# Kernel optimization log

Hardware: AMD Instinct MI355X
Metric: run time of the kernel (lower is better)

The kernel has to match this reference:

```python
import jax, jax.numpy as jnp
import numpy as np

EMBED_DIM = 1024
NUM_HEADS = 16
HEAD_DIM = EMBED_DIM // NUM_HEADS


def setup_inputs() -> dict:
    key = jax.random.key(0)
    k1, k2, k3, k4, k5 = jax.random.split(key, 5)
    B, T, C = 2, 2048, EMBED_DIM
    s = 1.0 / np.sqrt(C)
    return {
        "x": jax.random.normal(k1, (B, T, C), dtype=jnp.float32),
        "W_qkv": jax.random.normal(k2, (C, 3 * C), dtype=jnp.float32) * s,
        "b_qkv": jnp.zeros((3 * C,), dtype=jnp.float32),
        "W_out": jax.random.normal(k3, (C, C), dtype=jnp.float32) * s,
        "b_out": jnp.zeros((C,), dtype=jnp.float32),
    }


def reference(x, W_qkv, b_qkv, W_out, b_out):
    B, T, C = x.shape
    H, D = NUM_HEADS, HEAD_DIM
    qkv = x @ W_qkv + b_qkv                       # [B, T, 3C]
    q, k, v = jnp.split(qkv, 3, axis=-1)
    # [B, H, T, D]
    q = q.reshape(B, T, H, D).transpose(0, 2, 1, 3)
    k = k.reshape(B, T, H, D).transpose(0, 2, 1, 3)
    v = v.reshape(B, T, H, D).transpose(0, 2, 1, 3)
    scores = jnp.einsum("bhqd,bhkd->bhqk", q, k) / np.sqrt(D)  # [B,H,T,T]
    causal = jnp.tril(jnp.ones((T, T), dtype=bool))
    scores = jnp.where(causal[None, None], scores, -jnp.inf)
    weights = jax.nn.softmax(scores, axis=-1)
    out = jnp.einsum("bhqk,bhkd->bhqd", weights, v)  # [B,H,T,D]
    out = out.transpose(0, 2, 1, 3).reshape(B, T, C)
    return out @ W_out + b_out
```

## Files before the change

kernel.cpp:

```cpp
#include <hip/hip_runtime.h>
#include <stdint.h>

typedef unsigned short u16t;
typedef __attribute__((ext_vector_type(8))) short bf16x8;
typedef __attribute__((ext_vector_type(4))) float f32x4;

#define DEV __device__ __forceinline__

DEV u16t f2bf(float f) {
  union { float f; unsigned u; } v; v.f = f;
  unsigned r = v.u + 0x7FFFu + ((v.u >> 16) & 1u);
  return (u16t)(r >> 16);
}

DEV unsigned cvtpk(float a, float b) {
  unsigned r;
  asm("v_cvt_pk_bf16_f32 %0, %1, %2" : "=v"(r) : "v"(a), "v"(b));
  return r;
}

DEV void glds16(const void* g, void* l) {
  __builtin_amdgcn_global_load_lds((const __attribute__((address_space(1))) void*)g,
                                   (__attribute__((address_space(3))) void*)l, 16, 0, 0);
}

__global__ __launch_bounds__(256) void k_cast_x(const float* __restrict__ x,
                                                u16t* __restrict__ xb, int n) {
  int i = (blockIdx.x * 256 + threadIdx.x) * 8;
  if (i >= n) return;
  const float4* p = (const float4*)(x + i);
  float4 a = p[0], b = p[1];
  union { u16t h[8]; int4 v; } o;
  o.h[0] = f2bf(a.x); o.h[1] = f2bf(a.y); o.h[2] = f2bf(a.z); o.h[3] = f2bf(a.w);
  o.h[4] = f2bf(b.x); o.h[5] = f2bf(b.y); o.h[6] = f2bf(b.z); o.h[7] = f2bf(b.w);
  *(int4*)(xb + i) = o.v;
}

__global__ __launch_bounds__(256) void k_transpose_cast(const float* __restrict__ src,
                                                        u16t* __restrict__ dst,
                                                        int R, int C) {
  __shared__ u16t tile[64][65];
  int c0 = blockIdx.x * 64, r0 = blockIdx.y * 64;
  int tid = threadIdx.x;
#pragma unroll
  for (int i = 0; i < 16; i++) {
    int idx = tid + i * 256;
    int r = idx >> 6, c = idx & 63;
    tile[c][r] = f2bf(src[(size_t)(r0 + r) * C + (c0 + c)]);
  }
  __syncthreads();
#pragma unroll
  for (int i = 0; i < 16; i++) {
    int idx = tid + i * 256;
    int rr = idx >> 6, cc = idx & 63;
    dst[(size_t)(c0 + rr) * R + (r0 + cc)] = tile[rr][cc];
  }
}

template <int K>
DEV void gemm_mainloop(const u16t* __restrict__ A, const u16t* __restrict__ Bt,
                       int m0, int n0, u16t* ldsA, u16t* ldsB, f32x4 acc[4][4]) {
  const int tid = threadIdx.x;
  const int lane = tid & 63;
  const int wid = tid >> 6;
  const int wm = wid >> 1, wn = wid & 1;
#pragma unroll
  for (int i = 0; i < 4; i++)
#pragma unroll
    for (int j = 0; j < 4; j++) acc[i][j] = f32x4{0.f, 0.f, 0.f, 0.f};

  char* lA = (char*)ldsA;
  char* lB = (char*)ldsB;

  for (int k0 = 0; k0 < K; k0 += 32) {
#pragma unroll
    for (int j = 0; j < 2; j++) {
      int g = wid * 64 + lane + j * 256;
      int row = g >> 2;
      int cb = (g & 3) * 16;
      glds16((const char*)(A + (size_t)(m0 + row) * K + k0) + cb,
             lA + j * 4096 + wid * 1024);
      glds16((const char*)(Bt + (size_t)(n0 + row) * K + k0) + cb,
             lB + j * 4096 + wid * 1024);
    }
    __syncthreads();
    bf16x8 af[4], bfr[4];
    const int lr = lane & 15;
    const int ko = (lane >> 4) * 8;
#pragma unroll
    for (int f = 0; f < 4; f++) {
      af[f]  = *(const bf16x8*)(ldsA + (wm * 64 + f * 16 + lr) * 32 + ko);
      bfr[f] = *(const bf16x8*)(ldsB + (wn * 64 + f * 16 + lr) * 32 + ko);
    }
#pragma unroll
    for (int i = 0; i < 4; i++)
#pragma unroll
      for (int j = 0; j < 4; j++)
        acc[i][j] = __builtin_amdgcn_mfma_f32_16x16x32_bf16(af[i], bfr[j], acc[i][j], 0, 0, 0);
    __syncthreads();
  }
}

__global__ __launch_bounds__(256) void k_gemm_qkv(const u16t* __restrict__ xb,
                                                  const u16t* __restrict__ wt,
                                                  const float* __restrict__ bias,
                                                  u16t* __restrict__ q,
                                                  u16t* __restrict__ kk,
                                                  u16t* __restrict__ vt) {
  __shared__ u16t ldsA[128 * 32];
  __shared__ u16t ldsB[128 * 32];
  __shared__ u16t ldsE[4][64 * 64];
  const int m0 = blockIdx.x * 128, n0 = blockIdx.y * 128;
  f32x4 acc[4][4];
  gemm_mainloop<1024>(xb, wt, m0, n0, ldsA, ldsB, acc);

  const int lane = threadIdx.x & 63, wid = threadIdx.x >> 6;
  const int wm = wid >> 1, wn = wid & 1;
  const int nbase = n0 + wn * 64;
  const int which = nbase >> 10;
  const int hb = (nbase & 1023) >> 6;
  const int bb = m0 >> 11;
  const int t0 = (m0 & 2047) + wm * 64;
  const int bh = bb * 16 + hb;
  u16t* eb = ldsE[wid];
#pragma unroll
  for (int fm = 0; fm < 4; fm++) {
#pragma unroll
    for (int fn = 0; fn < 4; fn++) {
      float bv = bias[nbase + fn * 16 + (lane & 15)];
#pragma unroll
      for (int i = 0; i < 4; i++) {
        int t_loc = fm * 16 + (lane >> 4) * 4 + i;
        int d_loc = fn * 16 + (lane & 15);
        float v = acc[fm][fn][i] + bv;
        if (which == 2) eb[d_loc * 64 + t_loc] = f2bf(v);
        else            eb[t_loc * 64 + d_loc] = f2bf(v);
      }
    }
  }
  asm volatile("s_waitcnt lgkmcnt(0)" ::: "memory");
  u16t* dst;
  size_t base, rowstride;
  if (which == 2) { dst = vt; base = (size_t)bh * 64 * 2048 + t0; rowstride = 2048; }
  else { dst = (which == 0) ? q : kk; base = ((size_t)bh * 2048 + t0) * 64; rowstride = 64; }
#pragma unroll
  for (int it = 0; it < 8; it++) {
    int g = it * 64 + lane;
    int r = g >> 3;
    int ce = (g & 7) * 8;
    *(int4*)(dst + base + (size_t)r * rowstride + ce) = *(const int4*)(eb + r * 64 + ce);
  }
}

__global__ __launch_bounds__(128) void k_attn(const u16t* __restrict__ q,
                                              const u16t* __restrict__ kk,
                                              const u16t* __restrict__ vt,
                                              u16t* __restrict__ attn) {
  __shared__ u16t ldsK[64 * 64];
  __shared__ u16t ldsV[64 * 64];
  __shared__ u16t ldsP[2][16 * 64];
  const int p = blockIdx.x;
  const int t_lo = p, t_hi = 63 - p;
  const int lo_tiles = (t_lo >> 1) + 1;
  const int hi_tiles = (t_hi >> 1) + 1;
  const int bh = blockIdx.y;
  const int tid = threadIdx.x;
  const int lane = tid & 63, wid = tid >> 6;
  const int lr = lane & 15, lg = lane >> 4;
  const size_t hbase = (size_t)bh * 2048 * 64;
  const size_t vbase = (size_t)bh * 64 * 2048;
  const float NINF = -__builtin_inff();
  const float CEXP = 0.1803368801111204f;

  bf16x8 qlo[2], qhi[2];
  {
    const u16t* qp  = q + hbase + (size_t)(t_lo * 32 + wid * 16 + lr) * 64 + lg * 8;
    const u16t* qp2 = q + hbase + (size_t)(t_hi * 32 + wid * 16 + lr) * 64 + lg * 8;
#pragma unroll
    for (int ks = 0; ks < 2; ks++) {
      qlo[ks] = *(const bf16x8*)(qp + ks * 32);
      qhi[ks] = *(const bf16x8*)(qp2 + ks * 32);
    }
  }

  f32x4 olo[4], ohi[4];
#pragma unroll
  for (int i = 0; i < 4; i++) {
    olo[i] = f32x4{0.f, 0.f, 0.f, 0.f};
    ohi[i] = f32x4{0.f, 0.f, 0.f, 0.f};
  }
  float mlo = NINF, llo = 0.f, mhi = NINF, lhi = 0.f;

  u16t* pb = ldsP[wid];

  auto stage = [&](int kt) {
#pragma unroll
    for (int j = 0; j < 4; j++) {
      int g = j * 128 + tid;
      int r = g >> 3;
      int cb = (g & 7) * 16;
      int sc = cb ^ ((r & 7) << 4);
      glds16((const char*)(kk + hbase + (size_t)(kt * 64 + r) * 64) + sc,
             (char*)ldsK + j * 2048 + wid * 1024);
      glds16((const char*)(vt + vbase + (size_t)r * 2048 + kt * 64) + sc,
             (char*)ldsV + j * 2048 + wid * 1024);
    }
  };

  auto compute = [&](bool diag, int moff, const bf16x8* qf, f32x4* o,
                     float& m_run, float& l_run) {
    const char* K = (const char*)ldsK;
    const char* V = (const char*)ldsV;
    float sv[4][4];
    __builtin_amdgcn_s_setprio(1);
#pragma unroll
    for (int f = 0; f < 4; f++) {
      f32x4 s = f32x4{0.f, 0.f, 0.f, 0.f};
#pragma unroll
      for (int ks = 0; ks < 2; ks++) {
        int row = f * 16 + lr;
        int cb = ks * 64 + lg * 16;
        bf16x8 kf = *(const bf16x8*)(K + row * 128 + (cb ^ ((row & 7) << 4)));
        s = __builtin_amdgcn_mfma_f32_16x16x32_bf16(kf, qf[ks], s, 0, 0, 0);
      }
#pragma unroll
      for (int i = 0; i < 4; i++) sv[f][i] = s[i];
    }
    __builtin_amdgcn_s_setprio(0);
    if (diag) {
      int qr = moff + wid * 16 + lr;
#pragma unroll
      for (int f = 0; f < 4; f++)
#pragma unroll
        for (int i = 0; i < 4; i++)
          if (f * 16 + lg * 4 + i > qr) sv[f][i] = NINF;
    }
    float m0a = fmaxf(fmaxf(sv[0][0], sv[0][1]), fmaxf(sv[0][2], sv[0][3]));
    float m1a = fmaxf(fmaxf(sv[1][0], sv[1][1]), fmaxf(sv[1][2], sv[1][3]));
    float m2a = fmaxf(fmaxf(sv[2][0], sv[2][1]), fmaxf(sv[2][2], sv[2][3]));
    float m3a = fmaxf(fmaxf(sv[3][0], sv[3][1]), fmaxf(sv[3][2], sv[3][3]));
    float mx = fmaxf(fmaxf(m0a, m1a), fmaxf(m2a, m3a));
    mx = fmaxf(mx, __shfl_xor(mx, 16));
    mx = fmaxf(mx, __shfl_xor(mx, 32));
    if (!__all(mx <= m_run + 8.0f)) {
      float mnew = fmaxf(m_run, mx);
      float al = exp2f((m_run - mnew) * CEXP);
      m_run = mnew;
      l_run *= al;
#pragma unroll
      for (int df = 0; df < 4; df++)
#pragma unroll
        for (int i = 0; i < 4; i++) o[df][i] *= al;
    }
    const float nmc = -m_run * CEXP;
    float ps[4][4];
    float fs[4];
#pragma unroll
    for (int f = 0; f < 4; f++) {
#pragma unroll
      for (int i = 0; i < 4; i++)
        ps[f][i] = exp2f(__builtin_fmaf(sv[f][i], CEXP, nmc));
      fs[f] = (ps[f][0] + ps[f][1]) + (ps[f][2] + ps[f][3]);
    }
    float ssum = (fs[0] + fs[1]) + (fs[2] + fs[3]);
    ssum += __shfl_xor(ssum, 16);
    ssum += __shfl_xor(ssum, 32);
    l_run += ssum;
#pragma unroll
    for (int f = 0; f < 4; f++) {
      union { unsigned u[2]; uint2 v; } pk;
      pk.u[0] = cvtpk(ps[f][0], ps[f][1]);
      pk.u[1] = cvtpk(ps[f][2], ps[f][3]);
      int cby = (f * 32 + lg * 8) ^ ((lr & 7) << 4);
      *(uint2*)((char*)pb + lr * 128 + cby) = pk.v;
    }
    asm volatile("s_waitcnt lgkmcnt(0)" ::: "memory");
    __builtin_amdgcn_s_setprio(1);
#pragma unroll
    for (int ks = 0; ks < 2; ks++) {
      int cb = ks * 64 + lg * 16;
      bf16x8 pf = *(const bf16x8*)((const char*)pb + lr * 128 + (cb ^ ((lr & 7) << 4)));
#pragma unroll
      for (int df = 0; df < 4; df++) {
        int vrow = df * 16 + lr;
        bf16x8 vf = *(const bf16x8*)(V + vrow * 128 + (cb ^ ((vrow & 7) << 4)));
        o[df] = __builtin_amdgcn_mfma_f32_16x16x32_bf16(vf, pf, o[df], 0, 0, 0);
      }
    }
    __builtin_amdgcn_s_setprio(0);
  };

  for (int kt = 0; kt < hi_tiles; kt++) {
    stage(kt);
    __syncthreads();
    compute(kt == (t_hi >> 1), (t_hi & 1) << 5, qhi, ohi, mhi, lhi);
    if (kt < lo_tiles) compute(kt == (t_lo >> 1), (t_lo & 1) << 5, qlo, olo, mlo, llo);
    __syncthreads();
  }

  const int bb = bh >> 4, h = bh & 15;
  auto epi = [&](int qt, const f32x4* o, float l_run) {
    float rinv = 1.0f / l_run;
    int t = qt * 32 + wid * 16 + lr;
    size_t rowb = ((size_t)bb * 2048 + t) * 1024 + h * 64;
#pragma unroll
    for (int df = 0; df < 4; df++) {
      union { unsigned u[2]; uint2 v; } pk;
      pk.u[0] = cvtpk(o[df][0] * rinv, o[df][1] * rinv);
      pk.u[1] = cvtpk(o[df][2] * rinv, o[df][3] * rinv);
      *(uint2*)(attn + rowb + df * 16 + lg * 4) = pk.v;
    }
  };
  epi(t_lo, olo, llo);
  epi(t_hi, ohi, lhi);
}

__global__ __launch_bounds__(256) void k_gemm_out(const u16t* __restrict__ attn,
                                                  const u16t* __restrict__ wt,
                                                  const float* __restrict__ bias,
                                                  float* __restrict__ out) {
  __shared__ u16t ldsA[128 * 32];
  __shared__ u16t ldsB[128 * 32];
  const int m0 = blockIdx.x * 128, n0 = blockIdx.y * 128;
  f32x4 acc[4][4];
  gemm_mainloop<1024>(attn, wt, m0, n0, ldsA, ldsB, acc);

  const int lane = threadIdx.x & 63, wid = threadIdx.x >> 6;
  const int wm = wid >> 1, wn = wid & 1;
#pragma unroll
  for (int fm = 0; fm < 4; fm++) {
    int row = m0 + wm * 64 + fm * 16 + (lane >> 4) * 4;
#pragma unroll
    for (int fn = 0; fn < 4; fn++) {
      int col = n0 + wn * 64 + fn * 16 + (lane & 15);
      float bv = bias[col];
#pragma unroll
      for (int i = 0; i < 4; i++)
        out[(size_t)(row + i) * 1024 + col] = acc[fm][fn][i] + bv;
    }
  }
}

extern "C" void kernel_launch(void* const* d_in, const int* in_sizes, int n_in,
                              void* d_out, int out_size, void* d_ws, size_t ws_size,
                              hipStream_t stream) {
  const float* x     = (const float*)d_in[0];
  const float* W_qkv = (const float*)d_in[1];
  const float* b_qkv = (const float*)d_in[2];
  const float* W_out = (const float*)d_in[3];
  const float* b_out = (const float*)d_in[4];
  float* out = (float*)d_out;

  char* ws = (char*)d_ws;
  u16t* xb    = (u16t*)(ws);
  u16t* wqkvT = (u16t*)(ws + 8388608);
  u16t* woutT = (u16t*)(ws + 14680064);
  u16t* qb    = (u16t*)(ws + 16777216);
  u16t* kb    = (u16t*)(ws + 25165824);
  u16t* vtb   = (u16t*)(ws + 33554432);
  u16t* attnb = (u16t*)(ws + 41943040);

  k_cast_x<<<2048, 256, 0, stream>>>(x, xb, 4194304);
  k_transpose_cast<<<dim3(48, 16), 256, 0, stream>>>(W_qkv, wqkvT, 1024, 3072);
  k_transpose_cast<<<dim3(16, 16), 256, 0, stream>>>(W_out, woutT, 1024, 1024);
  k_gemm_qkv<<<dim3(32, 24), 256, 0, stream>>>(xb, wqkvT, b_qkv, qb, kb, vtb);
  k_attn<<<dim3(32, 32), 128, 0, stream>>>(qb, kb, vtb, attnb);
  k_gemm_out<<<dim3(32, 8), 256, 0, stream>>>(attnb, woutT, b_out, out);
}
```

Before: 132.5 us.

## Restructure attention into single-wave blocks loading K/V directly from global

The attention kernel now launches one 64-thread wave per 16-row query tile (128×32 grid) instead of 128-thread blocks processing paired lo/hi 32-row tiles. K and V fragments are read straight from global memory into registers rather than staged through LDS with barriers, which removes the __syncthreads and the async LDS copies. The cost is that K/V data is no longer shared between waves, so global/L2 traffic rises. The load-balancing pairing of short and long causal rows is also dropped, leaving the hardware scheduler to balance the uneven tile counts.

New measurement: 296.5 us. +123.9%, slower.

```diff
diff --git a/kernel.cpp b/kernel.cpp
--- a/kernel.cpp
+++ b/kernel.cpp
@@ -152,83 +152,63 @@
   }
 }
 
-__global__ __launch_bounds__(128) void k_attn(const u16t* __restrict__ q,
-                                              const u16t* __restrict__ kk,
-                                              const u16t* __restrict__ vt,
-                                              u16t* __restrict__ attn) {
-  __shared__ u16t ldsK[64 * 64];
-  __shared__ u16t ldsV[64 * 64];
-  __shared__ u16t ldsP[2][16 * 64];
-  const int p = blockIdx.x;
-  const int t_lo = p, t_hi = 63 - p;
-  const int lo_tiles = (t_lo >> 1) + 1;
-  const int hi_tiles = (t_hi >> 1) + 1;
+__global__ __launch_bounds__(64, 4) void k_attn(const u16t* __restrict__ q,
+                                                const u16t* __restrict__ kk,
+                                                const u16t* __restrict__ vt,
+                                                u16t* __restrict__ attn) {
+  __shared__ u16t ldsP[16 * 64];
+  const int qt = blockIdx.x;
   const int bh = blockIdx.y;
-  const int tid = threadIdx.x;
-  const int lane = tid & 63, wid = tid >> 6;
+  const int lane = threadIdx.x;
   const int lr = lane & 15, lg = lane >> 4;
+  const int ntiles = (qt >> 2) + 1;
+  const int moff = (qt & 3) << 4;
   const size_t hbase = (size_t)bh * 2048 * 64;
   const size_t vbase = (size_t)bh * 64 * 2048;
   const float NINF = -__builtin_inff();
   const float CEXP = 0.1803368801111204f;
 
-  bf16x8 qlo[2], qhi[2];
+  bf16x8 qf[2];
   {
-    const u16t* qp  = q + hbase + (size_t)(t_lo * 32 + wid * 16 + lr) * 64 + lg * 8;
-    const u16t* qp2 = q + hbase + (size_t)(t_hi * 32 + wid * 16 + lr) * 64 + lg * 8;
-#pragma unroll
-    for (int ks = 0; ks < 2; ks++) {
-      qlo[ks] = *(const bf16x8*)(qp + ks * 32);
-      qhi[ks] = *(const bf16x8*)(qp2 + ks * 32);
-    }
-  }
-
-  f32x4 olo[4], ohi[4];
-#pragma unroll
-  for (int i = 0; i < 4; i++) {
-    olo[i] = f32x4{0.f, 0.f, 0.f, 0.f};
-    ohi[i] = f32x4{0.f, 0.f, 0.f, 0.f};
-  }
-  float mlo = NINF, llo = 0.f, mhi = NINF, lhi = 0.f;
-
-  u16t* pb = ldsP[wid];
-
-  auto stage = [&](int kt) {
-#pragma unroll
-    for (int j = 0; j < 4; j++) {
-      int g = j * 128 + tid;
-      int r = g >> 3;
-      int cb = (g & 7) * 16;
-      int sc = cb ^ ((r & 7) << 4);
-      glds16((const char*)(kk + hbase + (size_t)(kt * 64 + r) * 64) + sc,
-             (char*)ldsK + j * 2048 + wid * 1024);
-      glds16((const char*)(vt + vbase + (size_t)r * 2048 + kt * 64) + sc,
-             (char*)ldsV + j * 2048 + wid * 1024);
-    }
-  };
-
-  auto compute = [&](bool diag, int moff, const bf16x8* qf, f32x4* o,
-                     float& m_run, float& l_run) {
-    const char* K = (const char*)ldsK;
-    const char* V = (const char*)ldsV;
+    const u16t* qp = q + hbase + (size_t)(qt * 16 + lr) * 64 + lg * 8;
+    qf[0] = *(const bf16x8*)(qp);
+    qf[1] = *(const bf16x8*)(qp + 32);
+  }
+
+  f32x4 o[4];
+#pragma unroll
+  for (int i = 0; i < 4; i++) o[i] = f32x4{0.f, 0.f, 0.f, 0.f};
+  float m_run = NINF, l_run = 0.f;
+
+  for (int kt = 0; kt < ntiles; kt++) {
+    const u16t* kp = kk + hbase + (size_t)kt * 64 * 64;
+    const u16t* vp = vt + vbase + kt * 64;
+    bf16x8 kf[4][2];
+#pragma unroll
+    for (int f = 0; f < 4; f++)
+#pragma unroll
+      for (int ks = 0; ks < 2; ks++)
+        kf[f][ks] = *(const bf16x8*)(kp + (f * 16 + lr) * 64 + ks * 32 + lg * 8);
+    bf16x8 vf[4][2];
+#pragma unroll
+    for (int df = 0; df < 4; df++)
+#pragma unroll
+      for (int ks = 0; ks < 2; ks++)
+        vf[df][ks] = *(const bf16x8*)(vp + (size_t)(df * 16 + lr) * 2048 + ks * 32 + lg * 8);
+
     float sv[4][4];
     __builtin_amdgcn_s_setprio(1);
 #pragma unroll
     for (int f = 0; f < 4; f++) {
       f32x4 s = f32x4{0.f, 0.f, 0.f, 0.f};
-#pragma unroll
-      for (int ks = 0; ks < 2; ks++) {
-        int row = f * 16 + lr;
-        int cb = ks * 64 + lg * 16;
-        bf16x8 kf = *(const bf16x8*)(K + row * 128 + (cb ^ ((row & 7) << 4)));
-        s = __builtin_amdgcn_mfma_f32_16x16x32_bf16(kf, qf[ks], s, 0, 0, 0);
-      }
+      s = __builtin_amdgcn_mfma_f32_16x16x32_bf16(kf[f][0], qf[0], s, 0, 0, 0);
+      s = __builtin_amdgcn_mfma_f32_16x16x32_bf16(kf[f][1], qf[1], s, 0, 0, 0);
 #pragma unroll
       for (int i = 0; i < 4; i++) sv[f][i] = s[i];
     }
     __builtin_amdgcn_s_setprio(0);
-    if (diag) {
-      int qr = moff + wid * 16 + lr;
+    if (kt == ntiles - 1) {
+      int qr = moff + lr;
 #pragma unroll
       for (int f = 0; f < 4; f++)
 #pragma unroll
@@ -272,47 +252,32 @@
       pk.u[0] = cvtpk(ps[f][0], ps[f][1]);
       pk.u[1] = cvtpk(ps[f][2], ps[f][3]);
       int cby = (f * 32 + lg * 8) ^ ((lr & 7) << 4);
-      *(uint2*)((char*)pb + lr * 128 + cby) = pk.v;
+      *(uint2*)((char*)ldsP + lr * 128 + cby) = pk.v;
     }
     asm volatile("s_waitcnt lgkmcnt(0)" ::: "memory");
     __builtin_amdgcn_s_setprio(1);
 #pragma unroll
     for (int ks = 0; ks < 2; ks++) {
       int cb = ks * 64 + lg * 16;
-      bf16x8 pf = *(const bf16x8*)((const char*)pb + lr * 128 + (cb ^ ((lr & 7) << 4)));
-#pragma unroll
-      for (int df = 0; df < 4; df++) {
-        int vrow = df * 16 + lr;
-        bf16x8 vf = *(const bf16x8*)(V + vrow * 128 + (cb ^ ((vrow & 7) << 4)));
-        o[df] = __builtin_amdgcn_mfma_f32_16x16x32_bf16(vf, pf, o[df], 0, 0, 0);
-      }
+      bf16x8 pf = *(const bf16x8*)((const char*)ldsP + lr * 128 + (cb ^ ((lr & 7) << 4)));
+#pragma unroll
+      for (int df = 0; df < 4; df++)
+        o[df] = __builtin_amdgcn_mfma_f32_16x16x32_bf16(vf[df][ks], pf, o[df], 0, 0, 0);
     }
     __builtin_amdgcn_s_setprio(0);
-  };
-
-  for (int kt = 0; kt < hi_tiles; kt++) {
-    stage(kt);
-    __syncthreads();
-    compute(kt == (t_hi >> 1), (t_hi & 1) << 5, qhi, ohi, mhi, lhi);
-    if (kt < lo_tiles) compute(kt == (t_lo >> 1), (t_lo & 1) << 5, qlo, olo, mlo, llo);
-    __syncthreads();
   }
 
   const int bb = bh >> 4, h = bh & 15;
-  auto epi = [&](int qt, const f32x4* o, float l_run) {
-    float rinv = 1.0f / l_run;
-    int t = qt * 32 + wid * 16 + lr;
-    size_t rowb = ((size_t)bb * 2048 + t) * 1024 + h * 64;
-#pragma unroll
-    for (int df = 0; df < 4; df++) {
-      union { unsigned u[2]; uint2 v; } pk;
-      pk.u[0] = cvtpk(o[df][0] * rinv, o[df][1] * rinv);
-      pk.u[1] = cvtpk(o[df][2] * rinv, o[df][3] * rinv);
-      *(uint2*)(attn + rowb + df * 16 + lg * 4) = pk.v;
-    }
-  };
-  epi(t_lo, olo, llo);
-  epi(t_hi, ohi, lhi);
+  float rinv = 1.0f / l_run;
+  int t = qt * 16 + lr;
+  size_t rowb = ((size_t)bb * 2048 + t) * 1024 + h * 64;
+#pragma unroll
+  for (int df = 0; df < 4; df++) {
+    union { unsigned u[2]; uint2 v; } pk;
+    pk.u[0] = cvtpk(o[df][0] * rinv, o[df][1] * rinv);
+    pk.u[1] = cvtpk(o[df][2] * rinv, o[df][3] * rinv);
+    *(uint2*)(attn + rowb + df * 16 + lg * 4) = pk.v;
+  }
 }
 
 __global__ __launch_bounds__(256) void k_gemm_out(const u16t* __restrict__ attn,
@@ -364,6 +329,6 @@
   k_transpose_cast<<<dim3(48, 16), 256, 0, stream>>>(W_qkv, wqkvT, 1024, 3072);
   k_transpose_cast<<<dim3(16, 16), 256, 0, stream>>>(W_out, woutT, 1024, 1024);
   k_gemm_qkv<<<dim3(32, 24), 256, 0, stream>>>(xb, wqkvT, b_qkv, qb, kb, vtb);
-  k_attn<<<dim3(32, 32), 128, 0, stream>>>(qb, kb, vtb, attnb);
+  k_attn<<<dim3(128, 32), 64, 0, stream>>>(qb, kb, vtb, attnb);
   k_gemm_out<<<dim3(32, 8), 256, 0, stream>>>(attnb, woutT, b_out, out);
 }
```
